# Kernel tuning notes

Measured on AMD Instinct MI355X. Metric: run time of the kernel, lower is better.

The kernel has to match this reference:

```python
import jax, jax.numpy as jnp
import numpy as np

NEG = -1000000.0  # mask value used by the original module


def setup_inputs() -> dict:
    key = jax.random.key(0)
    ks = jax.random.split(key, 8)
    N, D_IN, D_Q, D_K, E = 8192, 512, 512, 512, 262144
    s = 1.0 / np.sqrt(D_IN)
    return {
        "x": jax.random.normal(ks[0], (N, D_IN), dtype=jnp.float32),
        "edge_index": jax.random.randint(ks[1], (2, E), 0, N, dtype=jnp.int64),
        "Wq": jax.random.normal(ks[2], (D_IN, D_Q), dtype=jnp.float32) * s,
        "bq": jax.random.normal(ks[3], (D_Q,), dtype=jnp.float32) * 0.01,
        "Wk": jax.random.normal(ks[4], (D_IN, D_K), dtype=jnp.float32) * s,
        "bk": jax.random.normal(ks[5], (D_K,), dtype=jnp.float32) * 0.01,
        "Wv": jax.random.normal(ks[6], (D_IN, D_K), dtype=jnp.float32) * s,
        "bv": jax.random.normal(ks[7], (D_K,), dtype=jnp.float32) * 0.01,
    }


def reference(x, edge_index, Wq, bq, Wk, bk, Wv, bv):
    # Linear projections (x: [N, D_in])
    q = x @ Wq + bq  # [N, Dq]
    k = x @ Wk + bk  # [N, Dk]
    v = x @ Wv + bv  # [N, Dk]

    N = x.shape[0]
    # Dense adjacency from edge list (matches torch scatter adjacency[e0, e1] = 1)
    adj = jnp.zeros((N, N), dtype=x.dtype).at[edge_index[0], edge_index[1]].set(1.0)

    # Full scores (ptr=None branch), scaled by sqrt(Dq)
    a = (q @ k.T) / jnp.sqrt(jnp.asarray(q.shape[-1], dtype=x.dtype))
    a = a * adj + (1.0 - adj) * NEG

    attn = jax.nn.softmax(a, axis=-1)  # [N, N]
    return attn @ v  # [N, Dk]
```

## Files before the change

kernel.cpp:

```cpp
#include <hip/hip_runtime.h>


#define N_NODES 8192
#define DIM 512
#define MASK_WORDS 256
#define CAP 2048

typedef __attribute__((ext_vector_type(8))) short short8;
typedef __attribute__((ext_vector_type(4))) float f32x4;

__device__ __forceinline__ unsigned short f2bf(float f) {
    unsigned int u = __float_as_uint(f);
    u += 0x7fffu + ((u >> 16) & 1u);
    return (unsigned short)(u >> 16);
}
__device__ __forceinline__ float bf_lo(unsigned int w) { return __uint_as_float(w << 16); }
__device__ __forceinline__ float bf_hi(unsigned int w) { return __uint_as_float(w & 0xffff0000u); }

__global__ __launch_bounds__(256) void convert_x(const float* __restrict__ in,
                                                 unsigned short* __restrict__ outp, int n4)
{
    int i = blockIdx.x * 256 + threadIdx.x;
    if (i >= n4) return;
    float4 f = ((const float4*)in)[i];
    ushort4 o;
    o.x = f2bf(f.x); o.y = f2bf(f.y); o.z = f2bf(f.z); o.w = f2bf(f.w);
    ((ushort4*)outp)[i] = o;
}

__global__ __launch_bounds__(256) void convert_wT(
    const float* __restrict__ Wq, const float* __restrict__ Wk, const float* __restrict__ Wv,
    unsigned short* __restrict__ Wt)
{
    const int which = blockIdx.z;
    const float* __restrict__ W = (which == 0) ? Wq : (which == 1) ? Wk : Wv;
    unsigned short* __restrict__ outp = Wt + (size_t)which * DIM * DIM;

    __shared__ float t[32][33];
    const int k0 = blockIdx.y * 32, n0 = blockIdx.x * 32;
    const int tx = threadIdx.x & 31, ty = threadIdx.x >> 5;
    #pragma unroll
    for (int r = 0; r < 4; ++r)
        t[ty + 8 * r][tx] = W[(size_t)(k0 + ty + 8 * r) * DIM + n0 + tx];
    __syncthreads();
    #pragma unroll
    for (int r = 0; r < 4; ++r)
        outp[(size_t)(n0 + ty + 8 * r) * DIM + k0 + tx] = f2bf(t[tx][ty + 8 * r]);
}

__global__ __launch_bounds__(256) void mfma_gemm(
    const unsigned short* __restrict__ xb, const unsigned short* __restrict__ Wt,
    const float* __restrict__ bq, const float* __restrict__ bk, const float* __restrict__ bv,
    unsigned short* __restrict__ q, unsigned short* __restrict__ k, unsigned short* __restrict__ v)
{
    const int which = blockIdx.z;
    const unsigned short* __restrict__ Bm = Wt + (size_t)which * DIM * DIM;
    const float* __restrict__ bias = (which == 0) ? bq : (which == 1) ? bk : bv;
    unsigned short* __restrict__ outp = (which == 0) ? q : (which == 1) ? k : v;

    const int row0 = blockIdx.y * 128;
    const int col0 = blockIdx.x * 128;
    const int tid = threadIdx.x;
    const int lane = tid & 63;
    const int w = tid >> 6;
    const int wm = (w >> 1) * 64;
    const int wn = (w & 1) * 64;
    const int L = lane & 15;
    const int quad = lane >> 4;

    __shared__ unsigned short As[128 * 32];
    __shared__ unsigned short Bs[128 * 32];

    f32x4 zero = {0.f, 0.f, 0.f, 0.f};
    f32x4 acc[4][4];
    #pragma unroll
    for (int i = 0; i < 4; ++i)
        #pragma unroll
        for (int j = 0; j < 4; ++j) acc[i][j] = zero;

    for (int k0 = 0; k0 < DIM; k0 += 32) {
        #pragma unroll
        for (int c = 0; c < 2; ++c) {
            int ch = tid + c * 256;
            int m = ch >> 2, ko = (ch & 3) << 3;
            *(float4*)&As[m * 32 + ko] =
                *(const float4*)(const void*)(xb + (size_t)(row0 + m) * DIM + k0 + ko);
            *(float4*)&Bs[m * 32 + ko] =
                *(const float4*)(const void*)(Bm + (size_t)(col0 + m) * DIM + k0 + ko);
        }
        __syncthreads();

        short8 a[4], b[4];
        #pragma unroll
        for (int i = 0; i < 4; ++i)
            a[i] = *(const short8*)(const void*)&As[(wm + i * 16 + L) * 32 + quad * 8];
        #pragma unroll
        for (int j = 0; j < 4; ++j)
            b[j] = *(const short8*)(const void*)&Bs[(wn + j * 16 + L) * 32 + quad * 8];

        #pragma unroll
        for (int i = 0; i < 4; ++i)
            #pragma unroll
            for (int j = 0; j < 4; ++j)
                acc[i][j] = __builtin_amdgcn_mfma_f32_16x16x32_bf16(a[i], b[j], acc[i][j], 0, 0, 0);
        __syncthreads();
    }

    float biasv[4];
    #pragma unroll
    for (int j = 0; j < 4; ++j) biasv[j] = bias[col0 + wn + j * 16 + L];
    #pragma unroll
    for (int i = 0; i < 4; ++i) {
        int r0 = row0 + wm + i * 16 + quad * 4;
        #pragma unroll
        for (int j = 0; j < 4; ++j) {
            int c = col0 + wn + j * 16 + L;
            #pragma unroll
            for (int r = 0; r < 4; ++r)
                outp[(size_t)(r0 + r) * DIM + c] = f2bf(acc[i][j][r] + biasv[j]);
        }
    }
}

__global__ void build_mask(const int* __restrict__ ei,
                           unsigned int* __restrict__ mask, int E)
{
    int e = blockIdx.x * blockDim.x + threadIdx.x;
    if (e >= E) return;
    int src = ei[e];
    int dst = ei[E + e];
    atomicOr(&mask[(size_t)src * MASK_WORDS + (dst >> 5)], 1u << (dst & 31));
}

__global__ __launch_bounds__(256) void attn_kernel(
    const unsigned short* __restrict__ q, const unsigned short* __restrict__ k,
    const unsigned short* __restrict__ v, const unsigned int* __restrict__ mask,
    float* __restrict__ out)
{
    __shared__ unsigned short nbr[CAP];
    __shared__ float p_lds[CAP];
    __shared__ unsigned short q_s[DIM];
    __shared__ float redm[4], reds[4];
    __shared__ int redi[4];
    __shared__ int cnt;

    const int row = blockIdx.x;
    const int tid = threadIdx.x;
    const int lane = tid & 63;
    const int wid = tid >> 6;

    ((unsigned int*)q_s)[tid] = ((const unsigned int*)(q + (size_t)row * DIM))[tid];

    unsigned int mw = mask[(size_t)row * MASK_WORDS + tid];
    int pc = __popc(mw);
    #pragma unroll
    for (int off = 32; off >= 1; off >>= 1) pc += __shfl_down(pc, off, 64);
    if (lane == 0) redi[wid] = pc;
    __syncthreads();
    const int total = redi[0] + redi[1] + redi[2] + redi[3];

    if (total == 0) {
        float o0 = 0.f, o1 = 0.f;
        for (int j = 0; j < N_NODES; ++j) {
            unsigned int vv = ((const unsigned int*)(v + (size_t)j * DIM))[tid];
            o0 += bf_lo(vv); o1 += bf_hi(vv);
        }
        float2 res; res.x = o0 * (1.0f / N_NODES); res.y = o1 * (1.0f / N_NODES);
        ((float2*)(out + (size_t)row * DIM))[tid] = res;
        return;
    }

    const int nchunks = (total <= CAP) ? 1 : 4;
    const int wpc = (nchunks == 1) ? 256 : 64;

    float m_run = -3.0e38f, l_run = 0.f;
    float o0 = 0.f, o1 = 0.f;
    const float scale = 0.044194173824159220f;

    for (int c = 0; c < nchunks; ++c) {
        __syncthreads();
        if (tid == 0) cnt = 0;
        __syncthreads();
        if (tid < wpc) {
            unsigned int ww = mask[(size_t)row * MASK_WORDS + c * wpc + tid];
            while (ww) {
                int b = __ffs(ww) - 1; ww &= ww - 1;
                int pos = atomicAdd(&cnt, 1);
                nbr[pos] = (unsigned short)((c * wpc + tid) * 32 + b);
            }
        }
        __syncthreads();
        const int cn = cnt;
        if (cn == 0) continue;

        for (int p = wid; p < cn; p += 4) {
            const unsigned int* __restrict__ krow =
                (const unsigned int*)(k + (size_t)nbr[p] * DIM);
            float s = 0.f;
            #pragma unroll
            for (int t = 0; t < 4; ++t) {
                unsigned int kv = krow[lane + 64 * t];
                unsigned int qv = ((const unsigned int*)q_s)[lane + 64 * t];
                s += bf_lo(qv) * bf_lo(kv) + bf_hi(qv) * bf_hi(kv);
            }
            #pragma unroll
            for (int off = 32; off >= 1; off >>= 1) s += __shfl_down(s, off, 64);
            if (lane == 0) p_lds[p] = s * scale;
        }
        __syncthreads();

        float mc = -3.0e38f;
        for (int p = tid; p < cn; p += 256) mc = fmaxf(mc, p_lds[p]);
        #pragma unroll
        for (int off = 32; off >= 1; off >>= 1) mc = fmaxf(mc, __shfl_down(mc, off, 64));
        if (lane == 0) redm[wid] = mc;
        __syncthreads();
        mc = fmaxf(fmaxf(redm[0], redm[1]), fmaxf(redm[2], redm[3]));
        const float mnew = fmaxf(m_run, mc);
        const float f = __expf(m_run - mnew);

        float ls = 0.f;
        for (int p = tid; p < cn; p += 256) {
            float e = __expf(p_lds[p] - mnew);
            p_lds[p] = e;
            ls += e;
        }
        #pragma unroll
        for (int off = 32; off >= 1; off >>= 1) ls += __shfl_down(ls, off, 64);
        if (lane == 0) reds[wid] = ls;
        __syncthreads();
        l_run = l_run * f + (reds[0] + reds[1] + reds[2] + reds[3]);
        m_run = mnew;
        o0 *= f; o1 *= f;

        int p = 0;
        for (; p + 2 <= cn; p += 2) {
            const unsigned int* v0 = (const unsigned int*)(v + (size_t)nbr[p] * DIM);
            const unsigned int* v1 = (const unsigned int*)(v + (size_t)nbr[p + 1] * DIM);
            float w0 = p_lds[p], w1 = p_lds[p + 1];
            unsigned int a0 = v0[tid], a1 = v1[tid];
            o0 += w0 * bf_lo(a0) + w1 * bf_lo(a1);
            o1 += w0 * bf_hi(a0) + w1 * bf_hi(a1);
        }
        if (p < cn) {
            const unsigned int* v0 = (const unsigned int*)(v + (size_t)nbr[p] * DIM);
            float w0 = p_lds[p];
            unsigned int a0 = v0[tid];
            o0 += w0 * bf_lo(a0);
            o1 += w0 * bf_hi(a0);
        }
    }

    const float inv = 1.0f / l_run;
    float2 res; res.x = o0 * inv; res.y = o1 * inv;
    ((float2*)(out + (size_t)row * DIM))[tid] = res;
}

extern "C" void kernel_launch(void* const* d_in, const int* in_sizes, int n_in,
                              void* d_out, int out_size, void* d_ws, size_t ws_size,
                              hipStream_t stream)
{
    const float* x  = (const float*)d_in[0];
    const int*   ei = (const int*)d_in[1];
    const float* Wq = (const float*)d_in[2];
    const float* bq = (const float*)d_in[3];
    const float* Wk = (const float*)d_in[4];
    const float* bk = (const float*)d_in[5];
    const float* Wv = (const float*)d_in[6];
    const float* bv = (const float*)d_in[7];
    float* out = (float*)d_out;

    const int E = in_sizes[1] / 2;
    const size_t NM = (size_t)N_NODES * DIM;

    unsigned short* xb = (unsigned short*)d_ws;
    unsigned short* Wt = xb + NM;
    unsigned short* qb = Wt + (size_t)3 * DIM * DIM;
    unsigned short* kb = qb + NM;
    unsigned short* vb = kb + NM;
    unsigned int* mask = (unsigned int*)(vb + NM);

    hipMemsetAsync(mask, 0, (size_t)N_NODES * MASK_WORDS * sizeof(unsigned int), stream);

    convert_x<<<(int)(NM / 4 / 256), 256, 0, stream>>>(x, xb, (int)(NM / 4));
    convert_wT<<<dim3(16, 16, 3), 256, 0, stream>>>(Wq, Wk, Wv, Wt);
    build_mask<<<(E + 255) / 256, 256, 0, stream>>>(ei, mask, E);

    mfma_gemm<<<dim3(DIM / 128, N_NODES / 128, 3), 256, 0, stream>>>(
        xb, Wt, bq, bk, bv, qb, kb, vb);

    attn_kernel<<<N_NODES, 256, 0, stream>>>(qb, kb, vb, mask, out);
}
```

Baseline: 183.7 us.

## Merge prep kernels, use direct-to-LDS loads in GEMM, one row per wave in attention

Fuses the bf16 x conversion, weight transpose and adjacency mask build into one launch to cut launch overhead. The projection GEMM now stages tiles with global_load_lds instead of going through registers. The attention kernel maps one row per wavefront with 16-byte vector loads and wave-level shuffles, which removes the block-wide barriers and the under-used threads of the per-row-block design. The per-wave neighbor buffer is smaller, so rows with many neighbors take more chunks.

```diff
diff --git a/kernel.cpp b/kernel.cpp
--- a/kernel.cpp
+++ b/kernel.cpp
@@ -4,7 +4,7 @@
 #define N_NODES 8192
 #define DIM 512
 #define MASK_WORDS 256
-#define CAP 2048
+#define CAPW 512
 
 typedef __attribute__((ext_vector_type(8))) short short8;
 typedef __attribute__((ext_vector_type(4))) float f32x4;
@@ -17,35 +17,70 @@
 __device__ __forceinline__ float bf_lo(unsigned int w) { return __uint_as_float(w << 16); }
 __device__ __forceinline__ float bf_hi(unsigned int w) { return __uint_as_float(w & 0xffff0000u); }
 
-__global__ __launch_bounds__(256) void convert_x(const float* __restrict__ in,
-                                                 unsigned short* __restrict__ outp, int n4)
+__device__ __forceinline__ float wred_sum(float s) {
+    #pragma unroll
+    for (int off = 1; off <= 32; off <<= 1) s += __shfl_xor(s, off, 64);
+    return s;
+}
+__device__ __forceinline__ float wred_max(float s) {
+    #pragma unroll
+    for (int off = 1; off <= 32; off <<= 1) s = fmaxf(s, __shfl_xor(s, off, 64));
+    return s;
+}
+__device__ __forceinline__ int wred_sumi(int s) {
+    #pragma unroll
+    for (int off = 1; off <= 32; off <<= 1) s += __shfl_xor(s, off, 64);
+    return s;
+}
+__device__ __forceinline__ float dot8(uint4 a, uint4 b) {
+    return bf_lo(a.x) * bf_lo(b.x) + bf_hi(a.x) * bf_hi(b.x)
+         + bf_lo(a.y) * bf_lo(b.y) + bf_hi(a.y) * bf_hi(b.y)
+         + bf_lo(a.z) * bf_lo(b.z) + bf_hi(a.z) * bf_hi(b.z)
+         + bf_lo(a.w) * bf_lo(b.w) + bf_hi(a.w) * bf_hi(b.w);
+}
+
+__global__ __launch_bounds__(256) void prep(
+    const float* __restrict__ x, unsigned short* __restrict__ xb,
+    const float* __restrict__ Wq, const float* __restrict__ Wk,
+    const float* __restrict__ Wv, unsigned short* __restrict__ Wt,
+    const int* __restrict__ ei, unsigned int* __restrict__ mask, int E)
 {
-    int i = blockIdx.x * 256 + threadIdx.x;
-    if (i >= n4) return;
-    float4 f = ((const float4*)in)[i];
-    ushort4 o;
-    o.x = f2bf(f.x); o.y = f2bf(f.y); o.z = f2bf(f.z); o.w = f2bf(f.w);
-    ((ushort4*)outp)[i] = o;
-}
-
-__global__ __launch_bounds__(256) void convert_wT(
-    const float* __restrict__ Wq, const float* __restrict__ Wk, const float* __restrict__ Wv,
-    unsigned short* __restrict__ Wt)
-{
-    const int which = blockIdx.z;
-    const float* __restrict__ W = (which == 0) ? Wq : (which == 1) ? Wk : Wv;
-    unsigned short* __restrict__ outp = Wt + (size_t)which * DIM * DIM;
-
-    __shared__ float t[32][33];
-    const int k0 = blockIdx.y * 32, n0 = blockIdx.x * 32;
-    const int tx = threadIdx.x & 31, ty = threadIdx.x >> 5;
-    #pragma unroll
-    for (int r = 0; r < 4; ++r)
-        t[ty + 8 * r][tx] = W[(size_t)(k0 + ty + 8 * r) * DIM + n0 + tx];
-    __syncthreads();
-    #pragma unroll
-    for (int r = 0; r < 4; ++r)
-        outp[(size_t)(n0 + ty + 8 * r) * DIM + k0 + tx] = f2bf(t[tx][ty + 8 * r]);
+    __shared__ float sm[32][33];
+    const int b = blockIdx.x;
+    if (b < 4096) {
+        int i = b * 256 + threadIdx.x;
+        float4 f = ((const float4*)x)[i];
+        ushort4 o;
+        o.x = f2bf(f.x); o.y = f2bf(f.y); o.z = f2bf(f.z); o.w = f2bf(f.w);
+        ((ushort4*)xb)[i] = o;
+    } else if (b < 4864) {
+        int bb = b - 4096;
+        int which = bb >> 8, t = bb & 255;
+        const float* __restrict__ W = (which == 0) ? Wq : (which == 1) ? Wk : Wv;
+        unsigned short* __restrict__ outp = Wt + (size_t)which * DIM * DIM;
+        int n0 = (t & 15) * 32, k0 = (t >> 4) * 32;
+        int tx = threadIdx.x & 31, ty = threadIdx.x >> 5;
+        #pragma unroll
+        for (int r = 0; r < 4; ++r)
+            sm[ty + 8 * r][tx] = W[(size_t)(k0 + ty + 8 * r) * DIM + n0 + tx];
+        __syncthreads();
+        #pragma unroll
+        for (int r = 0; r < 4; ++r)
+            outp[(size_t)(n0 + ty + 8 * r) * DIM + k0 + tx] = f2bf(sm[tx][ty + 8 * r]);
+    } else {
+        int e = (b - 4864) * 256 + threadIdx.x;
+        if (e < E) {
+            int src = ei[e];
+            int dst = ei[E + e];
+            atomicOr(&mask[(size_t)src * MASK_WORDS + (dst >> 5)], 1u << (dst & 31));
+        }
+    }
+}
+
+__device__ __forceinline__ void load_lds16(const unsigned short* g, unsigned short* l) {
+    __builtin_amdgcn_global_load_lds(
+        (const __attribute__((address_space(1))) unsigned int*)g,
+        (__attribute__((address_space(3))) unsigned int*)l, 16, 0, 0);
 }
 
 __global__ __launch_bounds__(256) void mfma_gemm(
@@ -78,31 +113,29 @@
         #pragma unroll
         for (int j = 0; j < 4; ++j) acc[i][j] = zero;
 
+    const int m0 = tid >> 2;
+    const int ko = (tid & 3) << 3;
+
     for (int k0 = 0; k0 < DIM; k0 += 32) {
-        #pragma unroll
-        for (int c = 0; c < 2; ++c) {
-            int ch = tid + c * 256;
-            int m = ch >> 2, ko = (ch & 3) << 3;
-            *(float4*)&As[m * 32 + ko] =
-                *(const float4*)(const void*)(xb + (size_t)(row0 + m) * DIM + k0 + ko);
-            *(float4*)&Bs[m * 32 + ko] =
-                *(const float4*)(const void*)(Bm + (size_t)(col0 + m) * DIM + k0 + ko);
-        }
+        load_lds16(xb + (size_t)(row0 + m0) * DIM + k0 + ko,      As + tid * 8);
+        load_lds16(xb + (size_t)(row0 + 64 + m0) * DIM + k0 + ko, As + 2048 + tid * 8);
+        load_lds16(Bm + (size_t)(col0 + m0) * DIM + k0 + ko,      Bs + tid * 8);
+        load_lds16(Bm + (size_t)(col0 + 64 + m0) * DIM + k0 + ko, Bs + 2048 + tid * 8);
         __syncthreads();
 
-        short8 a[4], b[4];
+        short8 a[4], bfr[4];
         #pragma unroll
         for (int i = 0; i < 4; ++i)
             a[i] = *(const short8*)(const void*)&As[(wm + i * 16 + L) * 32 + quad * 8];
         #pragma unroll
         for (int j = 0; j < 4; ++j)
-            b[j] = *(const short8*)(const void*)&Bs[(wn + j * 16 + L) * 32 + quad * 8];
+            bfr[j] = *(const short8*)(const void*)&Bs[(wn + j * 16 + L) * 32 + quad * 8];
 
         #pragma unroll
         for (int i = 0; i < 4; ++i)
             #pragma unroll
             for (int j = 0; j < 4; ++j)
-                acc[i][j] = __builtin_amdgcn_mfma_f32_16x16x32_bf16(a[i], b[j], acc[i][j], 0, 0, 0);
+                acc[i][j] = __builtin_amdgcn_mfma_f32_16x16x32_bf16(a[i], bfr[j], acc[i][j], 0, 0, 0);
         __syncthreads();
     }
 
@@ -122,138 +155,129 @@
     }
 }
 
-__global__ void build_mask(const int* __restrict__ ei,
-                           unsigned int* __restrict__ mask, int E)
-{
-    int e = blockIdx.x * blockDim.x + threadIdx.x;
-    if (e >= E) return;
-    int src = ei[e];
-    int dst = ei[E + e];
-    atomicOr(&mask[(size_t)src * MASK_WORDS + (dst >> 5)], 1u << (dst & 31));
-}
-
 __global__ __launch_bounds__(256) void attn_kernel(
     const unsigned short* __restrict__ q, const unsigned short* __restrict__ k,
     const unsigned short* __restrict__ v, const unsigned int* __restrict__ mask,
     float* __restrict__ out)
 {
-    __shared__ unsigned short nbr[CAP];
-    __shared__ float p_lds[CAP];
-    __shared__ unsigned short q_s[DIM];
-    __shared__ float redm[4], reds[4];
-    __shared__ int redi[4];
-    __shared__ int cnt;
-
-    const int row = blockIdx.x;
+    __shared__ unsigned short nbr[4][CAPW];
+    __shared__ float pw[4][CAPW];
+    __shared__ int cnt[4];
+
     const int tid = threadIdx.x;
     const int lane = tid & 63;
     const int wid = tid >> 6;
-
-    ((unsigned int*)q_s)[tid] = ((const unsigned int*)(q + (size_t)row * DIM))[tid];
-
-    unsigned int mw = mask[(size_t)row * MASK_WORDS + tid];
-    int pc = __popc(mw);
-    #pragma unroll
-    for (int off = 32; off >= 1; off >>= 1) pc += __shfl_down(pc, off, 64);
-    if (lane == 0) redi[wid] = pc;
-    __syncthreads();
-    const int total = redi[0] + redi[1] + redi[2] + redi[3];
+    const int row = blockIdx.x * 4 + wid;
+
+    const uint4 qv = *(const uint4*)(q + (size_t)row * DIM + lane * 8);
+    const unsigned int* __restrict__ mrow = mask + (size_t)row * MASK_WORDS;
+
+    int pc = 0;
+    #pragma unroll
+    for (int t = 0; t < 4; ++t) pc += __popc(mrow[lane + 64 * t]);
+    const int total = wred_sumi(pc);
+
+    float o[8];
+    #pragma unroll
+    for (int i = 0; i < 8; ++i) o[i] = 0.f;
 
     if (total == 0) {
-        float o0 = 0.f, o1 = 0.f;
         for (int j = 0; j < N_NODES; ++j) {
-            unsigned int vv = ((const unsigned int*)(v + (size_t)j * DIM))[tid];
-            o0 += bf_lo(vv); o1 += bf_hi(vv);
-        }
-        float2 res; res.x = o0 * (1.0f / N_NODES); res.y = o1 * (1.0f / N_NODES);
-        ((float2*)(out + (size_t)row * DIM))[tid] = res;
+            uint4 vv = *(const uint4*)(v + (size_t)j * DIM + lane * 8);
+            o[0] += bf_lo(vv.x); o[1] += bf_hi(vv.x);
+            o[2] += bf_lo(vv.y); o[3] += bf_hi(vv.y);
+            o[4] += bf_lo(vv.z); o[5] += bf_hi(vv.z);
+            o[6] += bf_lo(vv.w); o[7] += bf_hi(vv.w);
+        }
+        float4 r0 = {o[0], o[1], o[2], o[3]};
+        float4 r1 = {o[4], o[5], o[6], o[7]};
+        const float s = 1.0f / N_NODES;
+        r0.x *= s; r0.y *= s; r0.z *= s; r0.w *= s;
+        r1.x *= s; r1.y *= s; r1.z *= s; r1.w *= s;
+        *(float4*)(out + (size_t)row * DIM + lane * 8) = r0;
+        *(float4*)(out + (size_t)row * DIM + lane * 8 + 4) = r1;
         return;
     }
 
-    const int nchunks = (total <= CAP) ? 1 : 4;
-    const int wpc = (nchunks == 1) ? 256 : 64;
+    const int nchunks = (total <= CAPW) ? 1 : 16;
+    const int wpc = (nchunks == 1) ? MASK_WORDS : 16;
+    const float scale = 0.044194173824159220f;
 
     float m_run = -3.0e38f, l_run = 0.f;
-    float o0 = 0.f, o1 = 0.f;
-    const float scale = 0.044194173824159220f;
 
     for (int c = 0; c < nchunks; ++c) {
-        __syncthreads();
-        if (tid == 0) cnt = 0;
-        __syncthreads();
-        if (tid < wpc) {
-            unsigned int ww = mask[(size_t)row * MASK_WORDS + c * wpc + tid];
+        if (lane == 0) cnt[wid] = 0;
+        for (int wi = lane; wi < wpc; wi += 64) {
+            unsigned int ww = mrow[c * wpc + wi];
             while (ww) {
-                int b = __ffs(ww) - 1; ww &= ww - 1;
-                int pos = atomicAdd(&cnt, 1);
-                nbr[pos] = (unsigned short)((c * wpc + tid) * 32 + b);
+                int bpos = __ffs(ww) - 1; ww &= ww - 1;
+                int pos = atomicAdd(&cnt[wid], 1);
+                nbr[wid][pos] = (unsigned short)((c * wpc + wi) * 32 + bpos);
             }
         }
-        __syncthreads();
-        const int cn = cnt;
+        const int cn = cnt[wid];
         if (cn == 0) continue;
 
-        for (int p = wid; p < cn; p += 4) {
-            const unsigned int* __restrict__ krow =
-                (const unsigned int*)(k + (size_t)nbr[p] * DIM);
-            float s = 0.f;
-            #pragma unroll
-            for (int t = 0; t < 4; ++t) {
-                unsigned int kv = krow[lane + 64 * t];
-                unsigned int qv = ((const unsigned int*)q_s)[lane + 64 * t];
-                s += bf_lo(qv) * bf_lo(kv) + bf_hi(qv) * bf_hi(kv);
+        for (int p = 0; p < cn; p += 2) {
+            int j0 = nbr[wid][p];
+            int j1 = nbr[wid][(p + 1 < cn) ? p + 1 : p];
+            uint4 k0v = *(const uint4*)(k + (size_t)j0 * DIM + lane * 8);
+            uint4 k1v = *(const uint4*)(k + (size_t)j1 * DIM + lane * 8);
+            float s0 = wred_sum(dot8(qv, k0v));
+            float s1 = wred_sum(dot8(qv, k1v));
+            if (lane == 0) {
+                pw[wid][p] = s0 * scale;
+                if (p + 1 < cn) pw[wid][p + 1] = s1 * scale;
             }
-            #pragma unroll
-            for (int off = 32; off >= 1; off >>= 1) s += __shfl_down(s, off, 64);
-            if (lane == 0) p_lds[p] = s * scale;
-        }
-        __syncthreads();
+        }
 
         float mc = -3.0e38f;
-        for (int p = tid; p < cn; p += 256) mc = fmaxf(mc, p_lds[p]);
-        #pragma unroll
-        for (int off = 32; off >= 1; off >>= 1) mc = fmaxf(mc, __shfl_down(mc, off, 64));
-        if (lane == 0) redm[wid] = mc;
-        __syncthreads();
-        mc = fmaxf(fmaxf(redm[0], redm[1]), fmaxf(redm[2], redm[3]));
+        for (int p = lane; p < cn; p += 64) mc = fmaxf(mc, pw[wid][p]);
+        mc = wred_max(mc);
         const float mnew = fmaxf(m_run, mc);
         const float f = __expf(m_run - mnew);
-
         float ls = 0.f;
-        for (int p = tid; p < cn; p += 256) {
-            float e = __expf(p_lds[p] - mnew);
-            p_lds[p] = e;
+        for (int p = lane; p < cn; p += 64) {
+            float e = __expf(pw[wid][p] - mnew);
+            pw[wid][p] = e;
             ls += e;
         }
-        #pragma unroll
-        for (int off = 32; off >= 1; off >>= 1) ls += __shfl_down(ls, off, 64);
-        if (lane == 0) reds[wid] = ls;
-        __syncthreads();
-        l_run = l_run * f + (reds[0] + reds[1] + reds[2] + reds[3]);
+        l_run = l_run * f + wred_sum(ls);
         m_run = mnew;
-        o0 *= f; o1 *= f;
+        #pragma unroll
+        for (int i = 0; i < 8; ++i) o[i] *= f;
 
         int p = 0;
         for (; p + 2 <= cn; p += 2) {
-            const unsigned int* v0 = (const unsigned int*)(v + (size_t)nbr[p] * DIM);
-            const unsigned int* v1 = (const unsigned int*)(v + (size_t)nbr[p + 1] * DIM);
-            float w0 = p_lds[p], w1 = p_lds[p + 1];
-            unsigned int a0 = v0[tid], a1 = v1[tid];
-            o0 += w0 * bf_lo(a0) + w1 * bf_lo(a1);
-            o1 += w0 * bf_hi(a0) + w1 * bf_hi(a1);
+            int j0 = nbr[wid][p], j1 = nbr[wid][p + 1];
+            float w0 = pw[wid][p], w1 = pw[wid][p + 1];
+            uint4 v0 = *(const uint4*)(v + (size_t)j0 * DIM + lane * 8);
+            uint4 v1 = *(const uint4*)(v + (size_t)j1 * DIM + lane * 8);
+            o[0] += w0 * bf_lo(v0.x) + w1 * bf_lo(v1.x);
+            o[1] += w0 * bf_hi(v0.x) + w1 * bf_hi(v1.x);
+            o[2] += w0 * bf_lo(v0.y) + w1 * bf_lo(v1.y);
+            o[3] += w0 * bf_hi(v0.y) + w1 * bf_hi(v1.y);
+            o[4] += w0 * bf_lo(v0.z) + w1 * bf_lo(v1.z);
+            o[5] += w0 * bf_hi(v0.z) + w1 * bf_hi(v1.z);
+            o[6] += w0 * bf_lo(v0.w) + w1 * bf_lo(v1.w);
+            o[7] += w0 * bf_hi(v0.w) + w1 * bf_hi(v1.w);
         }
         if (p < cn) {
-            const unsigned int* v0 = (const unsigned int*)(v + (size_t)nbr[p] * DIM);
-            float w0 = p_lds[p];
-            unsigned int a0 = v0[tid];
-            o0 += w0 * bf_lo(a0);
-            o1 += w0 * bf_hi(a0);
+            int j0 = nbr[wid][p];
+            float w0 = pw[wid][p];
+            uint4 v0 = *(const uint4*)(v + (size_t)j0 * DIM + lane * 8);
+            o[0] += w0 * bf_lo(v0.x); o[1] += w0 * bf_hi(v0.x);
+            o[2] += w0 * bf_lo(v0.y); o[3] += w0 * bf_hi(v0.y);
+            o[4] += w0 * bf_lo(v0.z); o[5] += w0 * bf_hi(v0.z);
+            o[6] += w0 * bf_lo(v0.w); o[7] += w0 * bf_hi(v0.w);
         }
     }
 
     const float inv = 1.0f / l_run;
-    float2 res; res.x = o0 * inv; res.y = o1 * inv;
-    ((float2*)(out + (size_t)row * DIM))[tid] = res;
+    float4 r0 = {o[0] * inv, o[1] * inv, o[2] * inv, o[3] * inv};
+    float4 r1 = {o[4] * inv, o[5] * inv, o[6] * inv, o[7] * inv};
+    *(float4*)(out + (size_t)row * DIM + lane * 8) = r0;
+    *(float4*)(out + (size_t)row * DIM + lane * 8 + 4) = r1;
 }
 
 extern "C" void kernel_launch(void* const* d_in, const int* in_sizes, int n_in,
@@ -282,12 +306,10 @@
 
     hipMemsetAsync(mask, 0, (size_t)N_NODES * MASK_WORDS * sizeof(unsigned int), stream);
 
-    convert_x<<<(int)(NM / 4 / 256), 256, 0, stream>>>(x, xb, (int)(NM / 4));
-    convert_wT<<<dim3(16, 16, 3), 256, 0, stream>>>(Wq, Wk, Wv, Wt);
-    build_mask<<<(E + 255) / 256, 256, 0, stream>>>(ei, mask, E);
+    prep<<<4864 + (E + 255) / 256, 256, 0, stream>>>(x, xb, Wq, Wk, Wv, Wt, ei, mask, E);
 
     mfma_gemm<<<dim3(DIM / 128, N_NODES / 128, 3), 256, 0, stream>>>(
         xb, Wt, bq, bk, bv, qb, kb, vb);
 
-    attn_kernel<<<N_NODES, 256, 0, stream>>>(qb, kb, vb, mask, out);
-}
+    attn_kernel<<<N_NODES / 4, 256, 0, stream>>>(qb, kb, vb, mask, out);
+}
```

Measured after the change: 173.1 us. 1.06x faster.
